# Kernel tuning notes

Measured on AMD Instinct MI355X. Metric: run time of the kernel, lower is better.

The kernel has to match this reference:

```python
import jax, jax.numpy as jnp
import numpy as np

B, N, C = 4, 2048, 1024
H = 16
D = C // H
FF = 4096
EPS = 1e-6


def _layernorm(x, g, b):
    mu = jnp.mean(x, axis=-1, keepdims=True)
    var = jnp.mean(jnp.square(x - mu), axis=-1, keepdims=True)
    return (x - mu) * jax.lax.rsqrt(var + EPS) * g + b


def setup_inputs() -> dict:
    key = jax.random.key(0)
    ks = jax.random.split(key, 8)
    s = 0.02
    x = jax.random.normal(ks[0], (B, N, C), dtype=jnp.float32)
    mask = jnp.tril(jnp.ones((N, N), dtype=bool))[None, None]  # causal [1,1,N,N]
    return {
        "x": x,
        "mask": mask,
        "qkv_w": jax.random.normal(ks[1], (3 * C, C), jnp.float32) * s,
        "qkv_b": jnp.zeros((3 * C,), jnp.float32),
        "proj_w": jax.random.normal(ks[2], (C, C), jnp.float32) * s,
        "proj_b": jnp.zeros((C,), jnp.float32),
        "ln1_g": jnp.ones((C,), jnp.float32),
        "ln1_b": jnp.zeros((C,), jnp.float32),
        "ln2_g": jnp.ones((C,), jnp.float32),
        "ln2_b": jnp.zeros((C,), jnp.float32),
        "w1": jax.random.normal(ks[3], (FF, C), jnp.float32) * s,
        "w2": jax.random.normal(ks[4], (C, FF), jnp.float32) * s,
        "w3": jax.random.normal(ks[5], (FF, C), jnp.float32) * s,
    }


def reference(x, mask, qkv_w, qkv_b, proj_w, proj_b, ln1_g, ln1_b, ln2_g, ln2_b, w1, w2, w3):
    # --- attention sub-block (pre-norm) ---
    h = _layernorm(x, ln1_g, ln1_b)
    qkv = h @ qkv_w.T + qkv_b                      # [B,N,3C]
    qkv = qkv.reshape(B, N, 3, H, D).transpose(2, 0, 3, 1, 4)  # [3,B,H,N,D]
    q, k, v = qkv[0], qkv[1], qkv[2]
    scale = D ** -0.5
    attn = jnp.einsum("bhnd,bhmd->bhnm", q, k) * scale
    attn = jnp.where(mask, attn, -jnp.inf)
    attn = jax.nn.softmax(attn, axis=-1)
    o = jnp.einsum("bhnm,bhmd->bhnd", attn, v)
    o = o.transpose(0, 2, 1, 3).reshape(B, N, C)
    o = o @ proj_w.T + proj_b
    x = x + o  # dropout is identity in eval mode
    # --- SwiGLU MLP sub-block (pre-norm) ---
    h = _layernorm(x, ln2_g, ln2_b)
    m = (jax.nn.silu(h @ w1.T) * (h @ w3.T)) @ w2.T
    return x + m
```

## Files before the change

### kernel.cpp

```cpp
#include <hip/hip_runtime.h>
#include <hip/hip_bf16.h>
#include <stdint.h>

#define NB   4
#define NSEQ 2048
#define NC   1024
#define NH   16
#define ND   64
#define NFF  4096
#define NM   (NB*NSEQ)

typedef __attribute__((ext_vector_type(8))) short short8v;
typedef __attribute__((ext_vector_type(4))) short short4v;
typedef __attribute__((ext_vector_type(4))) float f32x4;

#define GPTR(p) ((const __attribute__((address_space(1))) void*)(p))
#define LPTR(p) ((__attribute__((address_space(3))) void*)(p))

__device__ __forceinline__ short f2bf(float f){
  unsigned u = __builtin_bit_cast(unsigned, f);
  u += 0x7fffu + ((u >> 16) & 1u);
  return (short)(u >> 16);
}
__device__ __forceinline__ float bf2f(short h){
  unsigned u = ((unsigned)(unsigned short)h) << 16;
  return __builtin_bit_cast(float, u);
}
__device__ __forceinline__ f32x4 mfma16x32(short8v a, short8v b, f32x4 c){
  return __builtin_amdgcn_mfma_f32_16x16x32_bf16(a, b, c, 0, 0, 0);
}
__device__ __forceinline__ f32x4 mfma16x16(short4v a, short4v b, f32x4 c){
  return __builtin_amdgcn_mfma_f32_16x16x16bf16_1k(a, b, c, 0, 0, 0);
}
__device__ __forceinline__ short4v pack4bf(f32x4 v){
  __hip_bfloat162 a = __float22bfloat162_rn(float2{v[0], v[1]});
  __hip_bfloat162 b = __float22bfloat162_rn(float2{v[2], v[3]});
  short4v r;
  __builtin_memcpy(&r, &a, 4);
  __builtin_memcpy(((char*)&r) + 4, &b, 4);
  return r;
}

__global__ __launch_bounds__(256) void cvt_kernel(const float* __restrict__ w,
                                                  short* __restrict__ o, int n){
  int i = (blockIdx.x * 256 + threadIdx.x) * 4;
  if (i >= n) return;
  float4 v = *(const float4*)(w + i);
  short4v r = { f2bf(v.x), f2bf(v.y), f2bf(v.z), f2bf(v.w) };
  *(short4v*)(o + i) = r;
}

__global__ __launch_bounds__(256) void ln_kernel(const float* __restrict__ x,
                                                 const float* __restrict__ g,
                                                 const float* __restrict__ bta,
                                                 short* __restrict__ out){
  int row = blockIdx.x;
  int tid = threadIdx.x;
  int lane = tid & 63, w = tid >> 6;
  const float4* xr = (const float4*)(x + (size_t)row * NC);
  float4 v = xr[tid];
  float s1 = v.x + v.y + v.z + v.w;
  float s2 = v.x*v.x + v.y*v.y + v.z*v.z + v.w*v.w;
  #pragma unroll
  for (int off = 32; off; off >>= 1){
    s1 += __shfl_xor(s1, off);
    s2 += __shfl_xor(s2, off);
  }
  __shared__ float red[8];
  if (lane == 0){ red[w] = s1; red[4 + w] = s2; }
  __syncthreads();
  s1 = red[0] + red[1] + red[2] + red[3];
  s2 = red[4] + red[5] + red[6] + red[7];
  float mean = s1 * (1.0f / NC);
  float var  = s2 * (1.0f / NC) - mean * mean;
  float inv  = rsqrtf(var + 1e-6f);
  float4 gv = ((const float4*)g)[tid];
  float4 bv = ((const float4*)bta)[tid];
  short4v o = { f2bf((v.x - mean) * inv * gv.x + bv.x),
                f2bf((v.y - mean) * inv * gv.y + bv.y),
                f2bf((v.z - mean) * inv * gv.z + bv.z),
                f2bf((v.w - mean) * inv * gv.w + bv.w) };
  *(short4v*)(out + (size_t)row * NC + tid * 4) = o;
}

template<bool HAS_BIAS, bool HAS_RES, bool OUT_BF16, bool QKV_V>
__global__ __launch_bounds__(256, 3) void gemm_bt(const short* __restrict__ A,
                                                  const short* __restrict__ Bm,
                                                  const float* __restrict__ bias,
                                                  const float* __restrict__ res,
                                                  void* __restrict__ outp,
                                                  short* __restrict__ vt,
                                                  int Nc, int K){
  __shared__ short Al[128 * 64];
  __shared__ short Bl[128 * 64];
  int tid = threadIdx.x;
  int gx = gridDim.x, nwg = gx * gridDim.y;
  int wg = blockIdx.y * gx + blockIdx.x;
  int swz = (wg & 7) * (nwg >> 3) + (wg >> 3);
  int m0 = (swz / gx) * 128, n0 = (swz % gx) * 128;
  const short* Ag = A + (size_t)m0 * K;
  const short* Bg = Bm + (size_t)n0 * K;
  int lane = tid & 63, wid = tid >> 6;
  int wm = (wid >> 1) * 64, wn = (wid & 1) * 64;
  int qd = lane >> 4, l15 = lane & 15;

  f32x4 acc[4][4] = {};

  for (int k0 = 0; k0 < K; k0 += 64){
    __syncthreads();
    #pragma unroll
    for (int i = 0; i < 4; i++){
      int cg = (wid * 4 + i) * 64 + lane;
      int r  = cg >> 3, c = cg & 7;
      int sc = (c ^ (r & 7)) << 3;
      __builtin_amdgcn_global_load_lds(GPTR(Ag + (size_t)r * K + k0 + sc),
                                       LPTR(&Al[cg * 8]), 16, 0, 0);
      __builtin_amdgcn_global_load_lds(GPTR(Bg + (size_t)r * K + k0 + sc),
                                       LPTR(&Bl[cg * 8]), 16, 0, 0);
    }
    __syncthreads();
    #pragma unroll
    for (int kk = 0; kk < 2; kk++){
      short8v a[4], b[4];
      #pragma unroll
      for (int t = 0; t < 4; t++){
        int r = wm + t * 16 + l15;
        a[t] = *(const short8v*)&Al[r * 64 + (((kk * 4 + qd) ^ (r & 7)) << 3)];
      }
      #pragma unroll
      for (int t = 0; t < 4; t++){
        int r = wn + t * 16 + l15;
        b[t] = *(const short8v*)&Bl[r * 64 + (((kk * 4 + qd) ^ (r & 7)) << 3)];
      }
      #pragma unroll
      for (int i = 0; i < 4; i++)
        #pragma unroll
        for (int j = 0; j < 4; j++)
          acc[i][j] = mfma16x32(a[i], b[j], acc[i][j]);
    }
  }

  #pragma unroll
  for (int ti = 0; ti < 4; ti++){
    #pragma unroll
    for (int tj = 0; tj < 4; tj++){
      int col = n0 + wn + tj * 16 + l15;
      float bv = HAS_BIAS ? bias[col] : 0.0f;
      #pragma unroll
      for (int r = 0; r < 4; r++){
        int row = m0 + wm + ti * 16 + qd * 4 + r;
        float v = acc[ti][tj][r] + bv;
        if (QKV_V && col >= 2048){
          int hh = (col - 2048) >> 6, dd = col & 63;
          int bb = row >> 11, nn = row & 2047;
          vt[(((size_t)(bb * 16 + hh) * 64 + dd) << 11) + nn] = f2bf(v);
        } else {
          size_t idx = (size_t)row * Nc + col;
          if (HAS_RES) v += res[idx];
          if (OUT_BF16) ((short*)outp)[idx] = f2bf(v);
          else          ((float*)outp)[idx] = v;
        }
      }
    }
  }
}

__global__ __launch_bounds__(256, 2) void gemm_ff13(const short* __restrict__ A,
                                                    const short* __restrict__ B1m,
                                                    const short* __restrict__ B3m,
                                                    short* __restrict__ outp){
  __shared__ short Al [128 * 64];
  __shared__ short B1l[128 * 64];
  __shared__ short B3l[128 * 64];
  int tid = threadIdx.x;
  int gx = gridDim.x;
  int wg = blockIdx.y * gx + blockIdx.x;
  int xcd = wg & 7, idx = wg >> 3;
  int npx = gx >> 3;
  int n0 = (xcd * npx + idx % npx) * 128;
  int m0 = (idx / npx) * 128;
  const short* Ag  = A   + (size_t)m0 * NC;
  const short* B1g = B1m + (size_t)n0 * NC;
  const short* B3g = B3m + (size_t)n0 * NC;
  int lane = tid & 63, wid = tid >> 6;
  int wm = (wid >> 1) * 64, wn = (wid & 1) * 64;
  int qd = lane >> 4, l15 = lane & 15;

  f32x4 acc1[4][4] = {}, acc3[4][4] = {};

  for (int k0 = 0; k0 < NC; k0 += 64){
    __syncthreads();
    #pragma unroll
    for (int i = 0; i < 4; i++){
      int cg = (wid * 4 + i) * 64 + lane;
      int r  = cg >> 3, c = cg & 7;
      int sc = (c ^ (r & 7)) << 3;
      __builtin_amdgcn_global_load_lds(GPTR(Ag + (size_t)r * NC + k0 + sc),
                                       LPTR(&Al[cg * 8]), 16, 0, 0);
      __builtin_amdgcn_global_load_lds(GPTR(B1g + (size_t)r * NC + k0 + sc),
                                       LPTR(&B1l[cg * 8]), 16, 0, 0);
      __builtin_amdgcn_global_load_lds(GPTR(B3g + (size_t)r * NC + k0 + sc),
                                       LPTR(&B3l[cg * 8]), 16, 0, 0);
    }
    __syncthreads();
    #pragma unroll
    for (int kk = 0; kk < 2; kk++){
      short8v a[4], b1[4], b3[4];
      #pragma unroll
      for (int t = 0; t < 4; t++){
        int r = wm + t * 16 + l15;
        a[t] = *(const short8v*)&Al[r * 64 + (((kk * 4 + qd) ^ (r & 7)) << 3)];
      }
      #pragma unroll
      for (int t = 0; t < 4; t++){
        int r = wn + t * 16 + l15;
        int co = ((kk * 4 + qd) ^ (r & 7)) << 3;
        b1[t] = *(const short8v*)&B1l[r * 64 + co];
        b3[t] = *(const short8v*)&B3l[r * 64 + co];
      }
      #pragma unroll
      for (int i = 0; i < 4; i++)
        #pragma unroll
        for (int j = 0; j < 4; j++){
          acc1[i][j] = mfma16x32(a[i], b1[j], acc1[i][j]);
          acc3[i][j] = mfma16x32(a[i], b3[j], acc3[i][j]);
        }
    }
  }

  #pragma unroll
  for (int ti = 0; ti < 4; ti++){
    #pragma unroll
    for (int tj = 0; tj < 4; tj++){
      int col = n0 + wn + tj * 16 + l15;
      #pragma unroll
      for (int r = 0; r < 4; r++){
        int row = m0 + wm + ti * 16 + qd * 4 + r;
        float v1 = acc1[ti][tj][r];
        float v3 = acc3[ti][tj][r];
        float s = v1 / (1.0f + __expf(-v1)) * v3;
        outp[(size_t)row * NFF + col] = f2bf(s);
      }
    }
  }
}

__global__ __launch_bounds__(256) void attn_kernel(const short* __restrict__ qkvb,
                                                   const short* __restrict__ vt,
                                                   short* __restrict__ outb){
  const float QSCALE = 0.125f * 1.44269504f;
  int bh = blockIdx.x;
  int qb = 15 - blockIdx.y;
  int b = bh >> 4, h = bh & 15;
  int tid = threadIdx.x;
  int lane = tid & 63, wid = tid >> 6;
  int qd = lane >> 4, l15 = lane & 15;
  int qs = qb * 128 + wid * 32;

  const short* qbase = qkvb + (size_t)b * NSEQ * 3072 + h * 64;
  const short* kbase = qbase + 1024;
  const short* vtb   = vt + ((size_t)bh << 17);

  __shared__ short Kl[2][64 * 64];
  __shared__ short Vl[2][64 * 64];

  short8v qf[2][2];
  #pragma unroll
  for (int g = 0; g < 2; g++)
    #pragma unroll
    for (int kc = 0; kc < 2; kc++){
      short8v q = *(const short8v*)(qbase + (size_t)(qs + g * 16 + l15) * 3072
                                    + kc * 32 + qd * 8);
      short8v r;
      #pragma unroll
      for (int j = 0; j < 8; j++) r[j] = f2bf(bf2f(q[j]) * QSCALE);
      qf[g][kc] = r;
    }

  float l_i[2] = { 0.f, 0.f };
  f32x4 o[2][4];
  #pragma unroll
  for (int g = 0; g < 2; g++)
    #pragma unroll
    for (int t = 0; t < 4; t++)
      o[g][t] = (f32x4){0.f, 0.f, 0.f, 0.f};

  int nkt_blk = 2 * qb + 2;
  int itmax   = (qs + 31) >> 6;

  auto STAGE = [&](int bufi, int k0){
    #pragma unroll
    for (int i = 0; i < 2; i++){
      int cg = (wid * 2 + i) * 64 + lane;
      int r  = cg >> 3, c = cg & 7;
      int sc = (c ^ (r & 7)) << 3;
      __builtin_amdgcn_global_load_lds(GPTR(kbase + (size_t)(k0 + r) * 3072 + sc),
                                       LPTR(&Kl[bufi][cg * 8]), 16, 0, 0);
      __builtin_amdgcn_global_load_lds(GPTR(vtb + ((size_t)r << 11) + k0 + sc),
                                       LPTR(&Vl[bufi][cg * 8]), 16, 0, 0);
    }
  };

  STAGE(0, 0);
  __syncthreads();
  int cur = 0;

  for (int it = 0; it < nkt_blk; ++it){
    if (it + 1 < nkt_blk) STAGE(cur ^ 1, (it + 1) * 64);

    if (it <= itmax){
      int k0 = it * 64;
      short8v kf[4][2];
      #pragma unroll
      for (int kt = 0; kt < 4; kt++)
        #pragma unroll
        for (int kc = 0; kc < 2; kc++){
          int r = kt * 16 + l15;
          kf[kt][kc] = *(const short8v*)
              &Kl[cur][r * 64 + (((kc * 4 + qd) ^ (r & 7)) << 3)];
        }
      short4v vf[4][4];
      #pragma unroll
      for (int t = 0; t < 4; t++)
        #pragma unroll
        for (int ks = 0; ks < 4; ks++){
          int r = t * 16 + l15;
          vf[t][ks] = *(const short4v*)
              &Vl[cur][r * 64 + (((ks * 2 + (qd >> 1)) ^ (r & 7)) << 3)
                       + ((qd & 1) << 2)];
        }

      f32x4 s[2][4];
      #pragma unroll
      for (int g = 0; g < 2; g++)
        #pragma unroll
        for (int kt = 0; kt < 4; kt++){
          f32x4 z = (f32x4){0.f, 0.f, 0.f, 0.f};
          z = mfma16x32(kf[kt][0], qf[g][0], z);
          s[g][kt] = mfma16x32(kf[kt][1], qf[g][1], z);
        }

      if (it == itmax){
        #pragma unroll
        for (int g = 0; g < 2; g++){
          int qg = qs + g * 16 + l15;
          #pragma unroll
          for (int kt = 0; kt < 4; kt++)
            #pragma unroll
            for (int r = 0; r < 4; r++){
              int kg = k0 + kt * 16 + qd * 4 + r;
              s[g][kt][r] = (kg <= qg) ? s[g][kt][r] : -1e30f;
            }
        }
      }

      short4v pb[2][4];
      #pragma unroll
      for (int g = 0; g < 2; g++){
        #pragma unroll
        for (int kt = 0; kt < 4; kt++){
          f32x4 p;
          #pragma unroll
          for (int r = 0; r < 4; r++){
            float pv = exp2f(fminf(s[g][kt][r], 24.0f));
            p[r] = pv;
            l_i[g] += pv;
          }
          pb[g][kt] = pack4bf(p);
        }
      }

      #pragma unroll
      for (int g = 0; g < 2; g++)
        #pragma unroll
        for (int t = 0; t < 4; t++)
          #pragma unroll
          for (int ks = 0; ks < 4; ks++)
            o[g][t] = mfma16x16(vf[t][ks], pb[g][ks], o[g][t]);
    }

    __syncthreads();
    cur ^= 1;
  }

  #pragma unroll
  for (int g = 0; g < 2; g++){
    float l = l_i[g];
    l += __shfl_xor(l, 16);
    l += __shfl_xor(l, 32);
    float inv_l = 1.0f / l;
    int q = qs + g * 16 + l15;
    size_t rowbase = ((size_t)(b * NSEQ + q)) * NC + h * 64;
    #pragma unroll
    for (int t = 0; t < 4; t++){
      f32x4 v = { o[g][t][0] * inv_l, o[g][t][1] * inv_l,
                  o[g][t][2] * inv_l, o[g][t][3] * inv_l };
      *(short4v*)(outb + rowbase + t * 16 + qd * 4) = pack4bf(v);
    }
  }
}

extern "C" void kernel_launch(void* const* d_in, const int* in_sizes, int n_in,
                              void* d_out, int out_size, void* d_ws, size_t ws_size,
                              hipStream_t stream){
  const float* x      = (const float*)d_in[0];
  const float* qkv_w  = (const float*)d_in[2];
  const float* qkv_b  = (const float*)d_in[3];
  const float* proj_w = (const float*)d_in[4];
  const float* proj_b = (const float*)d_in[5];
  const float* ln1_g  = (const float*)d_in[6];
  const float* ln1_b  = (const float*)d_in[7];
  const float* ln2_g  = (const float*)d_in[8];
  const float* ln2_b  = (const float*)d_in[9];
  const float* w1     = (const float*)d_in[10];
  const float* w2     = (const float*)d_in[11];
  const float* w3     = (const float*)d_in[12];
  float* out = (float*)d_out;

  short* wqkv  = (short*)d_ws;
  short* wproj = wqkv  + (size_t)3072 * 1024;
  short* w1b   = wproj + (size_t)1024 * 1024;
  short* w3b   = w1b   + (size_t)4096 * 1024;
  short* w2b   = w3b   + (size_t)4096 * 1024;
  short* hb    = w2b   + (size_t)4096 * 1024;
  short* qkvb  = hb    + (size_t)NM * NC;
  short* attnb = qkvb  + (size_t)NM * 3072;
  short* ff3b  = attnb + (size_t)NM * NC;
  float* x1    = (float*)(ff3b + (size_t)NM * NFF);
  short* ff1b  = qkvb;
  short* vtb   = ff3b;

  cvt_kernel<<<3072 * 1024 / 1024, 256, 0, stream>>>(qkv_w, wqkv, 3072 * 1024);
  cvt_kernel<<<1024, 256, 0, stream>>>(proj_w, wproj, 1024 * 1024);
  cvt_kernel<<<4096, 256, 0, stream>>>(w1, w1b, 4096 * 1024);
  cvt_kernel<<<4096, 256, 0, stream>>>(w3, w3b, 4096 * 1024);
  cvt_kernel<<<4096, 256, 0, stream>>>(w2, w2b, 4096 * 1024);

  ln_kernel<<<NM, 256, 0, stream>>>(x, ln1_g, ln1_b, hb);
  gemm_bt<true, false, true, true><<<dim3(3072 / 128, NM / 128), 256, 0, stream>>>(
      hb, wqkv, qkv_b, nullptr, qkvb, vtb, 3072, 1024);
  attn_kernel<<<dim3(NB * NH, NSEQ / 128), 256, 0, stream>>>(qkvb, vtb, attnb);
  gemm_bt<true, true, false, false><<<dim3(1024 / 128, NM / 128), 256, 0, stream>>>(
      attnb, wproj, proj_b, x, x1, nullptr, 1024, 1024);
  ln_kernel<<<NM, 256, 0, stream>>>(x1, ln2_g, ln2_b, hb);
  gemm_ff13<<<dim3(4096 / 128, NM / 128), 256, 0, stream>>>(hb, w1b, w3b, ff1b);
  gemm_bt<false, true, false, false><<<dim3(1024 / 128, NM / 128), 256, 0, stream>>>(
      ff1b, w2b, nullptr, x1, out, nullptr, 1024, 4096);
}
```

Before: 554.1 us.

## Fuse weight casts with first LayerNorm, vectorize V stores, tune occupancy and priority

Merges the five weight fp32-to-bf16 conversion launches and the first LayerNorm into a single prep kernel, cutting launch overhead and letting those independent jobs run concurrently. The transposed V epilogue of the QKV GEMM now writes four bf16 values as one packed store instead of four scalar stores. The FF13 GEMM asks for 3 workgroups per CU instead of 2 through launch_bounds, which may force register spilling. The attention kernel raises wave priority around its MFMA blocks with s_setprio.

```diff
diff --git a/kernel.cpp b/kernel.cpp
--- a/kernel.cpp
+++ b/kernel.cpp
@@ -41,13 +41,55 @@
   return r;
 }
 
-__global__ __launch_bounds__(256) void cvt_kernel(const float* __restrict__ w,
-                                                  short* __restrict__ o, int n){
-  int i = (blockIdx.x * 256 + threadIdx.x) * 4;
-  if (i >= n) return;
-  float4 v = *(const float4*)(w + i);
-  short4v r = { f2bf(v.x), f2bf(v.y), f2bf(v.z), f2bf(v.w) };
-  *(short4v*)(o + i) = r;
+__global__ __launch_bounds__(256) void prep_kernel(
+    const float* __restrict__ qkv_w, const float* __restrict__ proj_w,
+    const float* __restrict__ w1, const float* __restrict__ w3,
+    const float* __restrict__ w2,
+    short* __restrict__ wqkv, short* __restrict__ wproj,
+    short* __restrict__ w1b, short* __restrict__ w3b, short* __restrict__ w2b,
+    const float* __restrict__ x, const float* __restrict__ g,
+    const float* __restrict__ bta, short* __restrict__ out){
+  int blk = blockIdx.x;
+  int tid = threadIdx.x;
+  if (blk < 16384){
+    const float* src; short* dst; int off;
+    if      (blk <  3072){ src = qkv_w;  dst = wqkv;  off = blk; }
+    else if (blk <  4096){ src = proj_w; dst = wproj; off = blk - 3072; }
+    else if (blk <  8192){ src = w1;     dst = w1b;   off = blk - 4096; }
+    else if (blk < 12288){ src = w3;     dst = w3b;   off = blk - 8192; }
+    else                 { src = w2;     dst = w2b;   off = blk - 12288; }
+    int i = (off * 256 + tid) * 4;
+    float4 v = *(const float4*)(src + i);
+    short4v r = { f2bf(v.x), f2bf(v.y), f2bf(v.z), f2bf(v.w) };
+    *(short4v*)(dst + i) = r;
+    return;
+  }
+  int row = blk - 16384;
+  int lane = tid & 63, w = tid >> 6;
+  const float4* xr = (const float4*)(x + (size_t)row * NC);
+  float4 v = xr[tid];
+  float s1 = v.x + v.y + v.z + v.w;
+  float s2 = v.x*v.x + v.y*v.y + v.z*v.z + v.w*v.w;
+  #pragma unroll
+  for (int off = 32; off; off >>= 1){
+    s1 += __shfl_xor(s1, off);
+    s2 += __shfl_xor(s2, off);
+  }
+  __shared__ float red[8];
+  if (lane == 0){ red[w] = s1; red[4 + w] = s2; }
+  __syncthreads();
+  s1 = red[0] + red[1] + red[2] + red[3];
+  s2 = red[4] + red[5] + red[6] + red[7];
+  float mean = s1 * (1.0f / NC);
+  float var  = s2 * (1.0f / NC) - mean * mean;
+  float inv  = rsqrtf(var + 1e-6f);
+  float4 gv = ((const float4*)g)[tid];
+  float4 bv = ((const float4*)bta)[tid];
+  short4v o = { f2bf((v.x - mean) * inv * gv.x + bv.x),
+                f2bf((v.y - mean) * inv * gv.y + bv.y),
+                f2bf((v.z - mean) * inv * gv.z + bv.z),
+                f2bf((v.w - mean) * inv * gv.w + bv.w) };
+  *(short4v*)(out + (size_t)row * NC + tid * 4) = o;
 }
 
 __global__ __launch_bounds__(256) void ln_kernel(const float* __restrict__ x,
@@ -146,15 +188,18 @@
     for (int tj = 0; tj < 4; tj++){
       int col = n0 + wn + tj * 16 + l15;
       float bv = HAS_BIAS ? bias[col] : 0.0f;
-      #pragma unroll
-      for (int r = 0; r < 4; r++){
-        int row = m0 + wm + ti * 16 + qd * 4 + r;
-        float v = acc[ti][tj][r] + bv;
-        if (QKV_V && col >= 2048){
-          int hh = (col - 2048) >> 6, dd = col & 63;
-          int bb = row >> 11, nn = row & 2047;
-          vt[(((size_t)(bb * 16 + hh) * 64 + dd) << 11) + nn] = f2bf(v);
-        } else {
+      if (QKV_V && col >= 2048){
+        int row0 = m0 + wm + ti * 16 + qd * 4;
+        int hh = (col - 2048) >> 6, dd = col & 63;
+        int bb = row0 >> 11, nn = row0 & 2047;
+        f32x4 v = { acc[ti][tj][0] + bv, acc[ti][tj][1] + bv,
+                    acc[ti][tj][2] + bv, acc[ti][tj][3] + bv };
+        *(short4v*)(vt + (((size_t)(bb * 16 + hh) * 64 + dd) << 11) + nn) = pack4bf(v);
+      } else {
+        #pragma unroll
+        for (int r = 0; r < 4; r++){
+          int row = m0 + wm + ti * 16 + qd * 4 + r;
+          float v = acc[ti][tj][r] + bv;
           size_t idx = (size_t)row * Nc + col;
           if (HAS_RES) v += res[idx];
           if (OUT_BF16) ((short*)outp)[idx] = f2bf(v);
@@ -165,7 +210,7 @@
   }
 }
 
-__global__ __launch_bounds__(256, 2) void gemm_ff13(const short* __restrict__ A,
+__global__ __launch_bounds__(256, 3) void gemm_ff13(const short* __restrict__ A,
                                                     const short* __restrict__ B1m,
                                                     const short* __restrict__ B3m,
                                                     short* __restrict__ outp){
@@ -331,6 +376,7 @@
         }
 
       f32x4 s[2][4];
+      __builtin_amdgcn_s_setprio(1);
       #pragma unroll
       for (int g = 0; g < 2; g++)
         #pragma unroll
@@ -339,6 +385,7 @@
           z = mfma16x32(kf[kt][0], qf[g][0], z);
           s[g][kt] = mfma16x32(kf[kt][1], qf[g][1], z);
         }
+      __builtin_amdgcn_s_setprio(0);
 
       if (it == itmax){
         #pragma unroll
@@ -370,6 +417,7 @@
         }
       }
 
+      __builtin_amdgcn_s_setprio(1);
       #pragma unroll
       for (int g = 0; g < 2; g++)
         #pragma unroll
@@ -377,6 +425,7 @@
           #pragma unroll
           for (int ks = 0; ks < 4; ks++)
             o[g][t] = mfma16x16(vf[t][ks], pb[g][ks], o[g][t]);
+      __builtin_amdgcn_s_setprio(0);
     }
 
     __syncthreads();
@@ -430,13 +479,9 @@
   short* ff1b  = qkvb;
   short* vtb   = ff3b;
 
-  cvt_kernel<<<3072 * 1024 / 1024, 256, 0, stream>>>(qkv_w, wqkv, 3072 * 1024);
-  cvt_kernel<<<1024, 256, 0, stream>>>(proj_w, wproj, 1024 * 1024);
-  cvt_kernel<<<4096, 256, 0, stream>>>(w1, w1b, 4096 * 1024);
-  cvt_kernel<<<4096, 256, 0, stream>>>(w3, w3b, 4096 * 1024);
-  cvt_kernel<<<4096, 256, 0, stream>>>(w2, w2b, 4096 * 1024);
-
-  ln_kernel<<<NM, 256, 0, stream>>>(x, ln1_g, ln1_b, hb);
+  prep_kernel<<<24576, 256, 0, stream>>>(qkv_w, proj_w, w1, w3, w2,
+                                         wqkv, wproj, w1b, w3b, w2b,
+                                         x, ln1_g, ln1_b, hb);
   gemm_bt<true, false, true, true><<<dim3(3072 / 128, NM / 128), 256, 0, stream>>>(
       hb, wqkv, qkv_b, nullptr, qkvb, vtb, 3072, 1024);
   attn_kernel<<<dim3(NB * NH, NSEQ / 128), 256, 0, stream>>>(qkvb, vtb, attnb);
```

After: 735.8 us. 1.33x slower.
